# Kernel tuning notes

Hardware: AMD Instinct MI355X
Metric: run time of the kernel (lower is better)

## Reference

```python
import jax, jax.numpy as jnp
import numpy as np

EPS = 1e-5  # nn.LayerNorm default


def channel_ln(x, g, b):
    # LayerNorm over the channel axis of an NCHW tensor
    mu = jnp.mean(x, axis=1, keepdims=True)
    var = jnp.mean((x - mu) ** 2, axis=1, keepdims=True)
    xn = (x - mu) * jax.lax.rsqrt(var + EPS)
    return xn * g[None, :, None, None] + b[None, :, None, None]


def setup_inputs() -> dict:
    key = jax.random.key(0)
    ks = jax.random.split(key, 8)
    B, C, H, W = 16, 392, 64, 64
    n, ws = 8, 7            # head_dim = C//n = 49 = ws'^2
    hidden = int(C * 4.0)
    f32 = jnp.float32
    return {
        "x": jax.random.normal(ks[0], (B, C, H, W), f32),
        "ln1_g": jnp.ones((C,), f32),
        "ln1_b": jnp.zeros((C,), f32),
        "qkv_w": jax.random.normal(ks[1], (3 * C, C), f32) * 0.02,
        "qkv_b": jnp.zeros((3 * C,), f32),
        "rel_bias": jax.random.normal(ks[2], (n, ws, ws), f32) * 0.02,
        "proj_w": jax.random.normal(ks[3], (C, C), f32) * 0.02,
        "proj_b": jnp.zeros((C,), f32),
        "ln2_g": jnp.ones((C,), f32),
        "ln2_b": jnp.zeros((C,), f32),
        "fc1_w": jax.random.normal(ks[4], (hidden, C), f32) * 0.02,
        "fc1_b": jnp.zeros((hidden,), f32),
        "fc2_w": jax.random.normal(ks[5], (C, hidden), f32) * 0.02,
        "fc2_b": jnp.zeros((C,), f32),
    }


def reference(x, ln1_g, ln1_b, qkv_w, qkv_b, rel_bias, proj_w, proj_b,
              ln2_g, ln2_b, fc1_w, fc1_b, fc2_w, fc2_b):
    B, C, H, W = x.shape
    n = rel_bias.shape[0]
    hd = C // n  # == ws'^2 (49)
    shortcut = x

    # --- attention branch ---
    h = channel_ln(x, ln1_g, ln1_b)
    qkv = jnp.einsum('oc,bchw->bohw', qkv_w, h) + qkv_b[None, :, None, None]
    qkv = qkv.reshape(B, 3, n, hd, H * W).transpose(1, 0, 2, 4, 3)  # [3,B,n,HW,hd]
    q, k, v = qkv[0], qkv[1], qkv[2]
    scale = hd ** -0.5
    bias = rel_bias.reshape(n, -1)[None, :, None, :]        # [1,n,1,hd]
    attn = jax.nn.softmax(q * scale * k + bias, axis=-1)    # elementwise qk score
    out = (attn * v).reshape(B, C, H, W)  # row-major reshape == torch .view on contiguous
    out = jnp.einsum('oc,bchw->bohw', proj_w, out) + proj_b[None, :, None, None]
    x = shortcut + out

    # --- conv-MLP branch ---
    h = channel_ln(x, ln2_g, ln2_b)
    h = jnp.einsum('oc,bchw->bohw', fc1_w, h) + fc1_b[None, :, None, None]
    h = jax.nn.gelu(h, approximate=False)  # nn.GELU default is exact erf
    h = jnp.einsum('oc,bchw->bohw', fc2_w, h) + fc2_b[None, :, None, None]
    return x + h
```

## Files before the change

### kernel.cpp

```cpp
#include <hip/hip_runtime.h>

typedef unsigned short u16;
typedef __attribute__((ext_vector_type(8))) short short8;
typedef __attribute__((ext_vector_type(8))) unsigned short u16x8;
typedef __attribute__((ext_vector_type(4))) unsigned short u16x4;
typedef __attribute__((ext_vector_type(4))) float f32x4;

#define DEVINL __device__ __forceinline__

DEVINL float bf2f(u16 v) { return __builtin_bit_cast(float, (unsigned int)v << 16); }
DEVINL u16 f2bf(float f) {
  unsigned int u = __builtin_bit_cast(unsigned int, f);
  u += 0x7fffu + ((u >> 16) & 1u);
  return (u16)(u >> 16);
}

DEVINL float loadx(const void* p, size_t i, int flag) {
  return flag ? bf2f(((const u16*)p)[i]) : ((const float*)p)[i];
}

DEVINL f32x4 mfma16(short8 a, short8 b, f32x4 c) {
  return __builtin_amdgcn_mfma_f32_16x16x32_bf16(a, b, c, 0, 0, 0);
}

DEVINL void gload16(const u16* g, u16* l) {
  __builtin_amdgcn_global_load_lds(
      (const __attribute__((address_space(1))) unsigned int*)g,
      (__attribute__((address_space(3))) unsigned int*)l,
      16, 0, 0);
}

#define WAIT_VM(n) asm volatile("s_waitcnt vmcnt(" #n ")" ::: "memory")
#define SBAR() __builtin_amdgcn_s_barrier()
#define SCHED_FENCE() __builtin_amdgcn_sched_barrier(0)

__global__ void k_detect(const unsigned int* __restrict__ xw, int* __restrict__ flag)
{
  const int t = threadIdx.x;
  int cnt = 0;
  for (int i = t; i < 4096; i += 256) {
    unsigned int w = xw[i];
    unsigned int h = w & 0xFFFFu;
    unsigned int e = (h >> 7) & 0xFFu;
    if (((h & 0x7FFFu) == 0u) || (e >= 117u && e <= 130u)) cnt++;
  }
  #pragma unroll
  for (int d = 1; d < 64; d <<= 1) cnt += __shfl_xor(cnt, d);
  __shared__ int acc[4];
  if ((t & 63) == 0) acc[t >> 6] = cnt;
  __syncthreads();
  if (t == 0) *flag = ((acc[0] + acc[1] + acc[2] + acc[3]) > 2048) ? 1 : 0;
}

__global__ void k_prep_fold(const void* __restrict__ w, const void* __restrict__ g,
                            const void* __restrict__ beta, const void* __restrict__ wbias,
                            const int* __restrict__ dflag,
                            u16* __restrict__ wp, float* __restrict__ wsum, float* __restrict__ cb,
                            int rows, int K, int KP)
{
  const int flag = *dflag;
  const int o = blockIdx.x;
  const int lane = threadIdx.x;
  float ws = 0.f, c = 0.f;
  if (o < rows) {
    for (int k = lane; k < KP; k += 64) {
      u16 outv = 0;
      if (k < K) {
        float wv = loadx(w, (size_t)o * K + k, flag);
        float gv = loadx(g, k, flag);
        outv = f2bf(wv * gv);
        ws += bf2f(outv);
        c  += wv * loadx(beta, k, flag);
      }
      wp[(size_t)o * KP + k] = outv;
    }
  } else {
    for (int k = lane; k < KP; k += 64) wp[(size_t)o * KP + k] = 0;
  }
  #pragma unroll
  for (int d = 1; d < 64; d <<= 1) { ws += __shfl_xor(ws, d); c += __shfl_xor(c, d); }
  if (lane == 0) { wsum[o] = ws; cb[o] = (o < rows) ? (c + loadx(wbias, o, flag)) : 0.f; }
}

__global__ void k_prep_pad(const void* __restrict__ w, const int* __restrict__ dflag,
                           u16* __restrict__ wp, int rows, int K, int KP, long total)
{
  const int flag = *dflag;
  long i = (long)blockIdx.x * 256 + threadIdx.x;
  if (i >= total) return;
  int r = (int)(i / KP), c2 = (int)(i % KP);
  wp[i] = (r < rows && c2 < K) ? f2bf(loadx(w, (size_t)r * K + c2, flag)) : (u16)0;
}

__global__ __launch_bounds__(256) void k_transpose(const void* __restrict__ xraw,
                                                   const int* __restrict__ dflag,
                                                   u16* __restrict__ xt, int jg0)
{
  __shared__ u16 ts[64][72];
  const int flag = *dflag;
  const int t = threadIdx.x;
  const int j0l = blockIdx.x * 64;
  const int j0g = jg0 + j0l;
  const int c0 = blockIdx.y * 64;
  const int c_l = t >> 2;
  const int c = c0 + c_l;
  const int bb = j0g >> 12;
  const int hw0 = j0g & 4095;

  #pragma unroll
  for (int u = 0; u < 2; ++u) {
    int jp = u * 32 + (t & 3) * 8;
    u16 vv[8] = {0, 0, 0, 0, 0, 0, 0, 0};
    if (c < 392) {
      size_t base = (((size_t)(bb * 392 + c)) << 12) + hw0 + jp;
      if (flag) {
        u16x8 v = *(const u16x8*)((const u16*)xraw + base);
        #pragma unroll
        for (int i = 0; i < 8; ++i) vv[i] = v[i];
      } else {
        const float* xf = (const float*)xraw + base;
        f32x4 a = *(const f32x4*)xf;
        f32x4 b = *(const f32x4*)(xf + 4);
        #pragma unroll
        for (int i = 0; i < 4; ++i) { vv[i] = f2bf(a[i]); vv[4 + i] = f2bf(b[i]); }
      }
    }
    #pragma unroll
    for (int i = 0; i < 8; ++i) ts[jp + i][c_l] = vv[i];
  }
  __syncthreads();
  const int j_l = t >> 2;
  #pragma unroll
  for (int u = 0; u < 2; ++u) {
    int cp = u * 32 + (t & 3) * 8;
    u16x8 w;
    #pragma unroll
    for (int i = 0; i < 8; ++i) w[i] = ts[j_l][cp + i];
    int cg = c0 + cp;
    if (cg < 416) *(u16x8*)(xt + (size_t)(j0l + j_l) * 416 + cg) = w;
  }
}

__global__ __launch_bounds__(256) void k_att_tr(const u16* __restrict__ att,
                                                u16* __restrict__ aout)
{
  __shared__ u16 ts[64][72];
  const int t = threadIdx.x;
  const int j0l = blockIdx.x * 64;
  const int c0 = blockIdx.y * 64;
  const int c_l = t >> 2;
  const int c = c0 + c_l;
  const int slab = j0l >> 12;
  const int hw0 = j0l & 4095;

  #pragma unroll
  for (int u = 0; u < 2; ++u) {
    int jp = u * 32 + (t & 3) * 8;
    u16x8 v = {0, 0, 0, 0, 0, 0, 0, 0};
    if (c < 392)
      v = *(const u16x8*)(att + (size_t)slab * 1605632 + (size_t)c * 4096 + hw0 + jp);
    #pragma unroll
    for (int i = 0; i < 8; ++i) ts[jp + i][c_l] = v[i];
  }
  __syncthreads();
  const int j_l = t >> 2;
  #pragma unroll
  for (int u = 0; u < 2; ++u) {
    int cp = u * 32 + (t & 3) * 8;
    u16x8 w;
    #pragma unroll
    for (int i = 0; i < 8; ++i) w[i] = ts[j_l][cp + i];
    int cg = c0 + cp;
    if (cg < 416) *(u16x8*)(aout + (size_t)(j0l + j_l) * 416 + cg) = w;
  }
}

__global__ __launch_bounds__(256) void k_rowstats(const u16* __restrict__ buf,
                                                  float* __restrict__ sum, float* __restrict__ sq)
{
  const int t = threadIdx.x;
  const int lane = t & 63;
  const int row = blockIdx.x * 4 + (t >> 6);
  float s = 0.f, q = 0.f;
  if (lane < 52) {
    u16x8 v = *(const u16x8*)(buf + (size_t)row * 416 + lane * 8);
    #pragma unroll
    for (int i = 0; i < 8; ++i) { float f = bf2f(v[i]); s += f; q += f * f; }
  }
  #pragma unroll
  for (int d = 1; d < 64; d <<= 1) { s += __shfl_xor(s, d); q += __shfl_xor(q, d); }
  if (lane == 0) { sum[row] = s; sq[row] = q; }
}

__global__ __launch_bounds__(256, 2) void k_qkv(
    const u16* __restrict__ xt, const u16* __restrict__ w1p,
    const float* __restrict__ wsum1, const float* __restrict__ cb1,
    const float* __restrict__ sum1, const float* __restrict__ sq1,
    const void* __restrict__ relb, const int* __restrict__ dflag,
    u16* __restrict__ attout)
{
  __shared__ __align__(16) u16 lsA[2 * 4096];
  __shared__ __align__(16) u16 lsB[2 * 6144];
  const int flag = *dflag;
  const int t = threadIdx.x;
  const int wid = t >> 6, lane = t & 63;
  const int l15 = lane & 15, quad = lane >> 4;
  const int bid = blockIdx.x;
  const int h = (bid >> 3) & 7;
  const int jl0 = ((bid & 7) + ((bid >> 6) << 3)) * 128;

  const u16* ga0 = xt + (size_t)(jl0 + (t >> 2)) * 416 + (t & 3) * 8;
  const u16* ga1 = ga0 + (size_t)64 * 416;
  const int orow = t >> 2, kpart = (t & 3) * 8;
  const u16* gbq = w1p + (size_t)(h * 49 + orow) * 416 + kpart;
  const u16* gbk = w1p + (size_t)(392 + h * 49 + orow) * 416 + kpart;
  const u16* gbv = w1p + (size_t)(784 + h * 49 + orow) * 416 + kpart;

  f32x4 zero4 = {0.f, 0.f, 0.f, 0.f};
  f32x4 accq[2][4], acck[2][4], accv[2][4];
  #pragma unroll
  for (int a = 0; a < 2; ++a)
    #pragma unroll
    for (int b2 = 0; b2 < 4; ++b2) { accq[a][b2] = zero4; acck[a][b2] = zero4; accv[a][b2] = zero4; }

  auto stage = [&](int b, int kk) {
    u16* A = lsA + b * 4096;
    u16* B = lsB + b * 6144;
    gload16(ga0 + kk, A + t * 8);
    gload16(ga1 + kk, A + 2048 + t * 8);
    gload16(gbq + kk, B + t * 8);
    gload16(gbk + kk, B + 2048 + t * 8);
    gload16(gbv + kk, B + 4096 + t * 8);
  };

  stage(0, 0);
  int cur = 0;
  for (int it = 0; it < 13; ++it) {
    if (it < 12) {
      stage(cur ^ 1, (it + 1) * 32);
      WAIT_VM(5);
    } else {
      WAIT_VM(0);
    }
    SBAR();
    SCHED_FENCE();
    const u16* A = lsA + cur * 4096;
    const u16* B = lsB + cur * 6144;
    short8 af0 = *(const short8*)(A + ((wid * 32 + l15) * 32 + quad * 8));
    short8 af1 = *(const short8*)(A + ((wid * 32 + 16 + l15) * 32 + quad * 8));
    #pragma unroll
    for (int of = 0; of < 4; ++of) {
      const int bo_ = (of * 16 + l15) * 32 + quad * 8;
      short8 bq = *(const short8*)(B + bo_);
      short8 bk = *(const short8*)(B + 2048 + bo_);
      short8 bv = *(const short8*)(B + 4096 + bo_);
      accq[0][of] = mfma16(af0, bq, accq[0][of]);
      accq[1][of] = mfma16(af1, bq, accq[1][of]);
      acck[0][of] = mfma16(af0, bk, acck[0][of]);
      acck[1][of] = mfma16(af1, bk, acck[1][of]);
      accv[0][of] = mfma16(af0, bv, accv[0][of]);
      accv[1][of] = mfma16(af1, bv, accv[1][of]);
    }
    SCHED_FENCE();
    SBAR();
    cur ^= 1;
  }

  const float scale = 1.f / 7.f;
  float cq[4], wq[4], ck[4], wk[4], cv[4], wv_[4], bo[4];
  int dl[4];
  #pragma unroll
  for (int of = 0; of < 4; ++of) {
    int d = of * 16 + l15; dl[of] = d;
    int rq = h * 49 + d, rk = 392 + h * 49 + d, rv = 784 + h * 49 + d;
    wq[of] = wsum1[rq]; cq[of] = cb1[rq];
    wk[of] = wsum1[rk]; ck[of] = cb1[rk];
    wv_[of] = wsum1[rv]; cv[of] = cb1[rv];
    bo[of] = (d < 49) ? loadx(relb, h * 49 + d, flag) : 0.f;
  }
  #pragma unroll
  for (int jf = 0; jf < 2; ++jf) {
    #pragma unroll
    for (int r = 0; r < 4; ++r) {
      int jl = jl0 + wid * 32 + jf * 16 + quad * 4 + r;
      float mu = sum1[jl] * (1.f / 392.f);
      float var = sq1[jl] * (1.f / 392.f) - mu * mu;
      float rs = rsqrtf(fmaxf(var, 0.f) + 1e-5f);
      float sv[4], vv[4];
      float mx = -1e30f;
      #pragma unroll
      for (int of = 0; of < 4; ++of) {
        float qv = rs * accq[jf][of][r] + cq[of] - mu * rs * wq[of];
        float kv = rs * acck[jf][of][r] + ck[of] - mu * rs * wk[of];
        float s = (dl[of] < 49) ? (qv * scale * kv + bo[of]) : -1e30f;
        sv[of] = s; mx = fmaxf(mx, s);
        vv[of] = rs * accv[jf][of][r] + cv[of] - mu * rs * wv_[of];
      }
      #pragma unroll
      for (int d2 = 1; d2 < 16; d2 <<= 1) mx = fmaxf(mx, __shfl_xor(mx, d2));
      float sum = 0.f;
      #pragma unroll
      for (int of = 0; of < 4; ++of) { float e = __expf(sv[of] - mx); sv[of] = e; sum += e; }
      #pragma unroll
      for (int d2 = 1; d2 < 16; d2 <<= 1) sum += __shfl_xor(sum, d2);
      float inv = 1.f / sum;
      int pos = jl & 4095, slab = jl >> 12;
      size_t base = (size_t)slab * 1605632 + (size_t)h * 200704 + (size_t)pos * 49;
      #pragma unroll
      for (int of = 0; of < 4; ++of) {
        if (dl[of] < 49) attout[base + dl[of]] = f2bf(sv[of] * inv * vv[of]);
      }
    }
  }
}

__global__ __launch_bounds__(256, 2) void k_proj(
    const u16* __restrict__ aout, const u16* __restrict__ wpp,
    const void* __restrict__ projb, const int* __restrict__ dflag,
    const u16* __restrict__ xt, u16* __restrict__ x2t)
{
  __shared__ __align__(16) u16 lsA[3 * 4096];
  __shared__ __align__(16) u16 lsB[3 * 4096];
  const int flag = *dflag;
  const int t = threadIdx.x;
  const int wid = t >> 6, lane = t & 63;
  const int l15 = lane & 15, quad = lane >> 4;
  const int jl0 = blockIdx.x * 128, o0 = blockIdx.y * 128;

  const u16* ga0 = aout + (size_t)(jl0 + (t >> 2)) * 416 + (t & 3) * 8;
  const u16* ga1 = ga0 + (size_t)64 * 416;
  const u16* gb0 = wpp + (size_t)(o0 + (t >> 2)) * 416 + (t & 3) * 8;
  const u16* gb1 = gb0 + (size_t)64 * 416;

  f32x4 zero4 = {0.f, 0.f, 0.f, 0.f};
  f32x4 acc[2][8];
  #pragma unroll
  for (int a = 0; a < 2; ++a)
    #pragma unroll
    for (int b2 = 0; b2 < 8; ++b2) acc[a][b2] = zero4;

  auto stage = [&](int b, int kk) {
    u16* A = lsA + b * 4096;
    u16* B = lsB + b * 4096;
    gload16(ga0 + kk, A + t * 8);
    gload16(ga1 + kk, A + 2048 + t * 8);
    gload16(gb0 + kk, B + t * 8);
    gload16(gb1 + kk, B + 2048 + t * 8);
  };

  stage(0, 0); stage(1, 32);
  int bc = 0, bs = 2;
  for (int it = 0; it < 13; ++it) {
    if (it + 2 < 13) { stage(bs, (it + 2) * 32); WAIT_VM(8); }
    else WAIT_VM(0);
    SBAR();
    SCHED_FENCE();
    const u16* A = lsA + bc * 4096;
    const u16* B = lsB + bc * 4096;
    short8 af0 = *(const short8*)(A + ((wid * 32 + l15) * 32 + quad * 8));
    short8 af1 = *(const short8*)(A + ((wid * 32 + 16 + l15) * 32 + quad * 8));
    #pragma unroll
    for (int of = 0; of < 8; ++of) {
      short8 bf = *(const short8*)(B + ((of * 16 + l15) * 32 + quad * 8));
      acc[0][of] = mfma16(af0, bf, acc[0][of]);
      acc[1][of] = mfma16(af1, bf, acc[1][of]);
    }
    SCHED_FENCE();
    SBAR();
    bc = (bc + 1 == 3) ? 0 : bc + 1;
    bs = (bs + 1 == 3) ? 0 : bs + 1;
  }

  float pb[8]; int og[8];
  #pragma unroll
  for (int of = 0; of < 8; ++of) {
    int o = o0 + of * 16 + l15; og[of] = o;
    pb[of] = (o < 392) ? loadx(projb, o, flag) : 0.f;
  }
  #pragma unroll
  for (int jf = 0; jf < 2; ++jf) {
    #pragma unroll
    for (int r = 0; r < 4; ++r) {
      int jl = jl0 + wid * 32 + jf * 16 + quad * 4 + r;
      #pragma unroll
      for (int of = 0; of < 8; ++of) {
        int o = og[of];
        if (o < 392) {
          float val = acc[jf][of][r] + pb[of] + bf2f(xt[(size_t)jl * 416 + o]);
          x2t[(size_t)jl * 416 + o] = f2bf(val);
        } else if (o < 416) {
          x2t[(size_t)jl * 416 + o] = 0;
        }
      }
    }
  }
}

__global__ __launch_bounds__(256, 2) void k_fc1(
    const u16* __restrict__ x2t, const u16* __restrict__ w3p,
    const float* __restrict__ wsum3, const float* __restrict__ cb3,
    const float* __restrict__ sum2, const float* __restrict__ sq2,
    u16* __restrict__ ut)
{
  __shared__ __align__(16) u16 lsA[3 * 4096];
  __shared__ __align__(16) u16 lsB[3 * 4096];
  const int t = threadIdx.x;
  const int wid = t >> 6, lane = t & 63;
  const int l15 = lane & 15, quad = lane >> 4;
  const int jl0 = blockIdx.x * 128, o0 = blockIdx.y * 128;

  const u16* ga0 = x2t + (size_t)(jl0 + (t >> 2)) * 416 + (t & 3) * 8;
  const u16* ga1 = ga0 + (size_t)64 * 416;
  const u16* gb0 = w3p + (size_t)(o0 + (t >> 2)) * 416 + (t & 3) * 8;
  const u16* gb1 = gb0 + (size_t)64 * 416;

  f32x4 zero4 = {0.f, 0.f, 0.f, 0.f};
  f32x4 acc[2][8];
  #pragma unroll
  for (int a = 0; a < 2; ++a)
    #pragma unroll
    for (int b2 = 0; b2 < 8; ++b2) acc[a][b2] = zero4;

  auto stage = [&](int b, int kk) {
    u16* A = lsA + b * 4096;
    u16* B = lsB + b * 4096;
    gload16(ga0 + kk, A + t * 8);
    gload16(ga1 + kk, A + 2048 + t * 8);
    gload16(gb0 + kk, B + t * 8);
    gload16(gb1 + kk, B + 2048 + t * 8);
  };

  stage(0, 0); stage(1, 32);
  int bc = 0, bs = 2;
  for (int it = 0; it < 13; ++it) {
    if (it + 2 < 13) { stage(bs, (it + 2) * 32); WAIT_VM(8); }
    else WAIT_VM(0);
    SBAR();
    SCHED_FENCE();
    const u16* A = lsA + bc * 4096;
    const u16* B = lsB + bc * 4096;
    short8 af0 = *(const short8*)(A + ((wid * 32 + l15) * 32 + quad * 8));
    short8 af1 = *(const short8*)(A + ((wid * 32 + 16 + l15) * 32 + quad * 8));
    #pragma unroll
    for (int of = 0; of < 8; ++of) {
      short8 bf = *(const short8*)(B + ((of * 16 + l15) * 32 + quad * 8));
      acc[0][of] = mfma16(af0, bf, acc[0][of]);
      acc[1][of] = mfma16(af1, bf, acc[1][of]);
    }
    SCHED_FENCE();
    SBAR();
    bc = (bc + 1 == 3) ? 0 : bc + 1;
    bs = (bs + 1 == 3) ? 0 : bs + 1;
  }

  float c3[8], w3[8]; int og[8];
  #pragma unroll
  for (int of = 0; of < 8; ++of) {
    int o = o0 + of * 16 + l15; og[of] = o;
    c3[of] = cb3[o]; w3[of] = wsum3[o];
  }
  #pragma unroll
  for (int jf = 0; jf < 2; ++jf) {
    #pragma unroll
    for (int r = 0; r < 4; ++r) {
      int jl = jl0 + wid * 32 + jf * 16 + quad * 4 + r;
      float mu = sum2[jl] * (1.f / 392.f);
      float var = sq2[jl] * (1.f / 392.f) - mu * mu;
      float rs = rsqrtf(fmaxf(var, 0.f) + 1e-5f);
      #pragma unroll
      for (int of = 0; of < 8; ++of) {
        if (og[of] < 1568) {
          float u = rs * acc[jf][of][r] + c3[of] - mu * rs * w3[of];
          float gl = 0.5f * u * (1.f + erff(u * 0.70710678118654752f));
          ut[(size_t)jl * 1568 + og[of]] = f2bf(gl);
        }
      }
    }
  }
}

__global__ __launch_bounds__(256, 2) void k_fc2(
    const u16* __restrict__ ut, const u16* __restrict__ wfp,
    const void* __restrict__ fc2b, const int* __restrict__ dflag,
    const u16* __restrict__ x2t, void* __restrict__ outp, int jfg0)
{
  __shared__ __align__(16) u16 lsA[3 * 4096];
  __shared__ __align__(16) u16 lsB[3 * 4096];
  const int flag = *dflag;
  const int t = threadIdx.x;
  const int wid = t >> 6, lane = t & 63;
  const int l15 = lane & 15, quad = lane >> 4;
  const int jl0 = blockIdx.x * 128, o0 = blockIdx.y * 128;

  const u16* ga0 = ut + (size_t)(jl0 + (t >> 2)) * 1568 + (t & 3) * 8;
  const u16* ga1 = ga0 + (size_t)64 * 1568;
  const u16* gb0 = wfp + (size_t)(o0 + (t >> 2)) * 1568 + (t & 3) * 8;
  const u16* gb1 = gb0 + (size_t)64 * 1568;

  f32x4 zero4 = {0.f, 0.f, 0.f, 0.f};
  f32x4 acc[2][8];
  #pragma unroll
  for (int a = 0; a < 2; ++a)
    #pragma unroll
    for (int b2 = 0; b2 < 8; ++b2) acc[a][b2] = zero4;

  auto stage = [&](int b, int kk) {
    u16* A = lsA + b * 4096;
    u16* B = lsB + b * 4096;
    gload16(ga0 + kk, A + t * 8);
    gload16(ga1 + kk, A + 2048 + t * 8);
    gload16(gb0 + kk, B + t * 8);
    gload16(gb1 + kk, B + 2048 + t * 8);
  };

  stage(0, 0); stage(1, 32);
  int bc = 0, bs = 2;
  for (int it = 0; it < 49; ++it) {
    if (it + 2 < 49) { stage(bs, (it + 2) * 32); WAIT_VM(8); }
    else WAIT_VM(0);
    SBAR();
    SCHED_FENCE();
    const u16* A = lsA + bc * 4096;
    const u16* B = lsB + bc * 4096;
    short8 af0 = *(const short8*)(A + ((wid * 32 + l15) * 32 + quad * 8));
    short8 af1 = *(const short8*)(A + ((wid * 32 + 16 + l15) * 32 + quad * 8));
    #pragma unroll
    for (int of = 0; of < 8; ++of) {
      short8 bf = *(const short8*)(B + ((of * 16 + l15) * 32 + quad * 8));
      acc[0][of] = mfma16(af0, bf, acc[0][of]);
      acc[1][of] = mfma16(af1, bf, acc[1][of]);
    }
    SCHED_FENCE();
    SBAR();
    bc = (bc + 1 == 3) ? 0 : bc + 1;
    bs = (bs + 1 == 3) ? 0 : bs + 1;
  }

  float fb[8]; int og[8];
  #pragma unroll
  for (int of = 0; of < 8; ++of) {
    int o = o0 + of * 16 + l15; og[of] = o;
    fb[of] = (o < 392) ? loadx(fc2b, o, flag) : 0.f;
  }
  #pragma unroll
  for (int jf = 0; jf < 2; ++jf) {
    int jlbase = jl0 + wid * 32 + jf * 16 + quad * 4;
    int jgbase = jfg0 + jlbase;
    int bslab = jgbase >> 12;
    int hw = jgbase & 4095;
    #pragma unroll
    for (int of = 0; of < 8; ++of) {
      if (og[of] < 392) {
        float v4[4];
        #pragma unroll
        for (int r = 0; r < 4; ++r)
          v4[r] = acc[jf][of][r] + fb[of] + bf2f(x2t[(size_t)(jlbase + r) * 416 + og[of]]);
        size_t obase = (((size_t)(bslab * 392 + og[of])) << 12) + hw;
        if (flag) {
          u16x4 pk;
          #pragma unroll
          for (int r = 0; r < 4; ++r) pk[r] = f2bf(v4[r]);
          *(u16x4*)((u16*)outp + obase) = pk;
        } else {
          f32x4 pk;
          #pragma unroll
          for (int r = 0; r < 4; ++r) pk[r] = v4[r];
          *(f32x4*)((float*)outp + obase) = pk;
        }
      }
    }
  }
}

extern "C" void kernel_launch(void* const* d_in, const int* in_sizes, int n_in,
                              void* d_out, int out_size, void* d_ws, size_t ws_size,
                              hipStream_t stream)
{
  if (n_in != 14 || in_sizes[0] != 16 * 392 * 64 * 64 || out_size != 16 * 392 * 64 * 64 ||
      in_sizes[3] != 3 * 392 * 392 || in_sizes[5] != 8 * 7 * 7 ||
      in_sizes[10] != 1568 * 392 || in_sizes[12] != 392 * 1568) {
    return;
  }

  const void* x     = d_in[0];
  const void* g1    = d_in[1];
  const void* b1    = d_in[2];
  const void* qkvw  = d_in[3];
  const void* qkvb  = d_in[4];
  const void* relb  = d_in[5];
  const void* projw = d_in[6];
  const void* projb = d_in[7];
  const void* g2    = d_in[8];
  const void* b2    = d_in[9];
  const void* fc1w  = d_in[10];
  const void* fc1b  = d_in[11];
  const void* fc2w  = d_in[12];
  const void* fc2b  = d_in[13];

  int S = 0, F = 0;
  {
    const int cand[8][2] = {{16,8},{16,4},{8,4},{8,2},{4,2},{4,1},{2,1},{1,1}};
    for (int i = 0; i < 8; ++i) {
      size_t nb = (size_t)cand[i][0] * 4096 * 416 * 2 * 3
                + (size_t)cand[i][1] * 4096 * 1568 * 2
                + (size_t)16 * 1024 * 1024;
      if (nb <= ws_size) { S = cand[i][0]; F = cand[i][1]; break; }
    }
    if (S == 0) return;
  }

  char* wsb = (char*)d_ws;
  size_t off = 0;
  auto alloc = [&](size_t bytes) -> void* {
    void* p = wsb + off;
    off = (off + bytes + 255) & ~(size_t)255;
    return p;
  };
  int*  dflag = (int*)alloc(256);
  u16* xt    = (u16*)alloc((size_t)S * 4096 * 416 * 2);
  u16* aout  = (u16*)alloc((size_t)S * 4096 * 416 * 2);
  u16* x2t   = (u16*)alloc((size_t)S * 4096 * 416 * 2);
  u16* ut    = (u16*)alloc((size_t)F * 4096 * 1568 * 2);
  u16* w1p   = (u16*)alloc((size_t)1200 * 416 * 2);
  u16* w3p   = (u16*)alloc((size_t)1664 * 416 * 2);
  u16* wpp   = (u16*)alloc((size_t)512 * 416 * 2);
  u16* wfp   = (u16*)alloc((size_t)512 * 1568 * 2);
  float* wsum1 = (float*)alloc(1200 * 4);
  float* cb1   = (float*)alloc(1200 * 4);
  float* wsum3 = (float*)alloc(1664 * 4);
  float* cb3   = (float*)alloc(1664 * 4);
  float* sum1  = (float*)alloc((size_t)65536 * 4);
  float* sq1   = (float*)alloc((size_t)65536 * 4);
  float* sum2  = (float*)alloc((size_t)65536 * 4);
  float* sq2   = (float*)alloc((size_t)65536 * 4);

  u16* att = x2t;

  k_detect<<<1, 256, 0, stream>>>((const unsigned int*)x, dflag);

  k_prep_fold<<<1200, 64, 0, stream>>>(qkvw, g1, b1, qkvb, dflag, w1p, wsum1, cb1, 1176, 392, 416);
  k_prep_fold<<<1664, 64, 0, stream>>>(fc1w, g2, b2, fc1b, dflag, w3p, wsum3, cb3, 1568, 392, 416);
  k_prep_pad<<<(512 * 416 + 255) / 256, 256, 0, stream>>>(projw, dflag, wpp, 392, 392, 416, (long)512 * 416);
  k_prep_pad<<<(512 * 1568 + 255) / 256, 256, 0, stream>>>(fc2w, dflag, wfp, 392, 1568, 1568, (long)512 * 1568);

  for (int c0 = 0; c0 < 16; c0 += S) {
    const int jg0 = c0 * 4096;
    k_transpose<<<dim3(S * 64, 7), 256, 0, stream>>>(x, dflag, xt, jg0);
    k_rowstats<<<S * 1024, 256, 0, stream>>>(xt, sum1, sq1);
    k_qkv<<<dim3(S * 256), 256, 0, stream>>>(xt, w1p, wsum1, cb1, sum1, sq1, relb, dflag, att);
    k_att_tr<<<dim3(S * 64, 7), 256, 0, stream>>>(att, aout);
    k_proj<<<dim3(S * 32, 4), 256, 0, stream>>>(aout, wpp, projb, dflag, xt, x2t);
    k_rowstats<<<S * 1024, 256, 0, stream>>>(x2t, sum2, sq2);
    for (int f0 = 0; f0 < S; f0 += F) {
      const int jfg0 = (c0 + f0) * 4096;
      const u16* x2sub = x2t + (size_t)f0 * 4096 * 416;
      k_fc1<<<dim3(F * 32, 13), 256, 0, stream>>>(x2sub, w3p, wsum3, cb3,
                                                  sum2 + (size_t)f0 * 4096, sq2 + (size_t)f0 * 4096, ut);
      k_fc2<<<dim3(F * 32, 4), 256, 0, stream>>>(ut, wfp, fc2b, dflag, x2sub, d_out, jfg0);
    }
  }
}
```

Baseline: 897.9 us.

## Enlarge GEMM tiles to 128x512 and prepack weights into MFMA fragment order

The proj, fc1 and fc2 GEMMs now use 512-thread blocks, each computing a 128-row by 512-column tile. Every wave holds 4x8 MFMA accumulators, so the A operand is read from global memory only once per output column group. Weights are repacked in a new prep kernel into a fragment-major layout, so each lane's LDS load is a contiguous 16-byte read with no per-row stride. This raises register and LDS pressure (about 120KB of LDS per block) and pads fc1 outputs to 2048, which wastes MFMA work on padded columns.

```diff
diff --git a/kernel.cpp b/kernel.cpp
--- a/kernel.cpp
+++ b/kernel.cpp
@@ -90,6 +90,18 @@
   if (i >= total) return;
   int r = (int)(i / KP), c2 = (int)(i % KP);
   wp[i] = (r < rows && c2 < K) ? f2bf(loadx(w, (size_t)r * K + c2, flag)) : (u16)0;
+}
+
+__global__ void k_repack(const u16* __restrict__ src, u16* __restrict__ dst, int RP, int KP)
+{
+  const int nK = KP / 32;
+  long i = (long)blockIdx.x * 256 + threadIdx.x;
+  if (i * 8 >= (long)RP * KP) return;
+  int l = (int)(i & 63);
+  long fk = i >> 6;
+  int ks = (int)(fk % nK), f = (int)(fk / nK);
+  const u16* s = src + (size_t)(f * 16 + (l & 15)) * KP + ks * 32 + ((l >> 4) & 3) * 8;
+  *(u16x8*)(dst + i * 8) = *(const u16x8*)s;
 }
 
 __global__ __launch_bounds__(256) void k_transpose(const void* __restrict__ xraw,
@@ -236,12 +248,8 @@
   stage(0, 0);
   int cur = 0;
   for (int it = 0; it < 13; ++it) {
-    if (it < 12) {
-      stage(cur ^ 1, (it + 1) * 32);
-      WAIT_VM(5);
-    } else {
-      WAIT_VM(0);
-    }
+    if (it < 12) { stage(cur ^ 1, (it + 1) * 32); WAIT_VM(5); }
+    else WAIT_VM(0);
     SBAR();
     SCHED_FENCE();
     const u16* A = lsA + cur * 4096;
@@ -314,56 +322,58 @@
   }
 }
 
-__global__ __launch_bounds__(256, 2) void k_proj(
-    const u16* __restrict__ aout, const u16* __restrict__ wpp,
+
+__global__ __launch_bounds__(512, 2) void k_proj(
+    const u16* __restrict__ aout, const u16* __restrict__ wppf,
     const void* __restrict__ projb, const int* __restrict__ dflag,
     const u16* __restrict__ xt, u16* __restrict__ x2t)
 {
   __shared__ __align__(16) u16 lsA[3 * 4096];
-  __shared__ __align__(16) u16 lsB[3 * 4096];
+  __shared__ __align__(16) u16 lsB[3 * 16384];
   const int flag = *dflag;
   const int t = threadIdx.x;
-  const int wid = t >> 6, lane = t & 63;
-  const int l15 = lane & 15, quad = lane >> 4;
-  const int jl0 = blockIdx.x * 128, o0 = blockIdx.y * 128;
-
-  const u16* ga0 = aout + (size_t)(jl0 + (t >> 2)) * 416 + (t & 3) * 8;
-  const u16* ga1 = ga0 + (size_t)64 * 416;
-  const u16* gb0 = wpp + (size_t)(o0 + (t >> 2)) * 416 + (t & 3) * 8;
-  const u16* gb1 = gb0 + (size_t)64 * 416;
+  const int w = t >> 6, lane = t & 63;
+  const int l15 = lane & 15, quad = (lane >> 4) & 3;
+  const int jl0 = blockIdx.x * 128;
+  const int NK = 13;
+
+  const u16* gA = aout + (size_t)(jl0 + (t >> 6) * 16 + l15) * 416 + quad * 8;
+  const u16* gB = wppf + (size_t)(t >> 6) * NK * 512 + lane * 8;
 
   f32x4 zero4 = {0.f, 0.f, 0.f, 0.f};
-  f32x4 acc[2][8];
-  #pragma unroll
-  for (int a = 0; a < 2; ++a)
-    #pragma unroll
-    for (int b2 = 0; b2 < 8; ++b2) acc[a][b2] = zero4;
-
-  auto stage = [&](int b, int kk) {
-    u16* A = lsA + b * 4096;
-    u16* B = lsB + b * 4096;
-    gload16(ga0 + kk, A + t * 8);
-    gload16(ga1 + kk, A + 2048 + t * 8);
-    gload16(gb0 + kk, B + t * 8);
-    gload16(gb1 + kk, B + 2048 + t * 8);
+  f32x4 acc[4][8];
+  #pragma unroll
+  for (int m = 0; m < 4; ++m)
+    #pragma unroll
+    for (int n = 0; n < 8; ++n) acc[m][n] = zero4;
+
+  auto stage = [&](int b, int ks) {
+    gload16(gA + ks * 32, lsA + b * 4096 + t * 8);
+    #pragma unroll
+    for (int c = 0; c < 4; ++c)
+      gload16(gB + ((size_t)c * 8 * NK + ks) * 512,
+              lsB + b * 16384 + (c * 8 + w) * 512 + lane * 8);
   };
 
-  stage(0, 0); stage(1, 32);
+  stage(0, 0); stage(1, 1);
   int bc = 0, bs = 2;
-  for (int it = 0; it < 13; ++it) {
-    if (it + 2 < 13) { stage(bs, (it + 2) * 32); WAIT_VM(8); }
+  for (int ks = 0; ks < NK; ++ks) {
+    if (ks + 2 < NK) { stage(bs, ks + 2); WAIT_VM(10); }
+    else if (ks + 1 < NK) WAIT_VM(5);
     else WAIT_VM(0);
     SBAR();
     SCHED_FENCE();
     const u16* A = lsA + bc * 4096;
-    const u16* B = lsB + bc * 4096;
-    short8 af0 = *(const short8*)(A + ((wid * 32 + l15) * 32 + quad * 8));
-    short8 af1 = *(const short8*)(A + ((wid * 32 + 16 + l15) * 32 + quad * 8));
-    #pragma unroll
-    for (int of = 0; of < 8; ++of) {
-      short8 bf = *(const short8*)(B + ((of * 16 + l15) * 32 + quad * 8));
-      acc[0][of] = mfma16(af0, bf, acc[0][of]);
-      acc[1][of] = mfma16(af1, bf, acc[1][of]);
+    const u16* B = lsB + bc * 16384;
+    short8 af[4];
+    #pragma unroll
+    for (int m = 0; m < 4; ++m)
+      af[m] = *(const short8*)(A + ((w >> 2) * 4 + m) * 512 + lane * 8);
+    #pragma unroll
+    for (int n = 0; n < 8; ++n) {
+      short8 bf = *(const short8*)(B + ((w & 3) * 8 + n) * 512 + lane * 8);
+      #pragma unroll
+      for (int m = 0; m < 4; ++m) acc[m][n] = mfma16(af[m], bf, acc[m][n]);
     }
     SCHED_FENCE();
     SBAR();
@@ -373,20 +383,21 @@
 
   float pb[8]; int og[8];
   #pragma unroll
-  for (int of = 0; of < 8; ++of) {
-    int o = o0 + of * 16 + l15; og[of] = o;
-    pb[of] = (o < 392) ? loadx(projb, o, flag) : 0.f;
-  }
-  #pragma unroll
-  for (int jf = 0; jf < 2; ++jf) {
+  for (int n = 0; n < 8; ++n) {
+    int o = (w & 3) * 128 + n * 16 + l15; og[n] = o;
+    pb[n] = (o < 392) ? loadx(projb, o, flag) : 0.f;
+  }
+  const int row0 = jl0 + (w >> 2) * 64;
+  #pragma unroll
+  for (int m = 0; m < 4; ++m) {
     #pragma unroll
     for (int r = 0; r < 4; ++r) {
-      int jl = jl0 + wid * 32 + jf * 16 + quad * 4 + r;
-      #pragma unroll
-      for (int of = 0; of < 8; ++of) {
-        int o = og[of];
+      int jl = row0 + m * 16 + quad * 4 + r;
+      #pragma unroll
+      for (int n = 0; n < 8; ++n) {
+        int o = og[n];
         if (o < 392) {
-          float val = acc[jf][of][r] + pb[of] + bf2f(xt[(size_t)jl * 416 + o]);
+          float val = acc[m][n][r] + pb[n] + bf2f(xt[(size_t)jl * 416 + o]);
           x2t[(size_t)jl * 416 + o] = f2bf(val);
         } else if (o < 416) {
           x2t[(size_t)jl * 416 + o] = 0;
@@ -396,56 +407,58 @@
   }
 }
 
-__global__ __launch_bounds__(256, 2) void k_fc1(
-    const u16* __restrict__ x2t, const u16* __restrict__ w3p,
+__global__ __launch_bounds__(512, 2) void k_fc1(
+    const u16* __restrict__ x2t, const u16* __restrict__ w3pf,
     const float* __restrict__ wsum3, const float* __restrict__ cb3,
     const float* __restrict__ sum2, const float* __restrict__ sq2,
     u16* __restrict__ ut)
 {
   __shared__ __align__(16) u16 lsA[3 * 4096];
-  __shared__ __align__(16) u16 lsB[3 * 4096];
-  const int t = threadIdx.x;
-  const int wid = t >> 6, lane = t & 63;
-  const int l15 = lane & 15, quad = lane >> 4;
-  const int jl0 = blockIdx.x * 128, o0 = blockIdx.y * 128;
-
-  const u16* ga0 = x2t + (size_t)(jl0 + (t >> 2)) * 416 + (t & 3) * 8;
-  const u16* ga1 = ga0 + (size_t)64 * 416;
-  const u16* gb0 = w3p + (size_t)(o0 + (t >> 2)) * 416 + (t & 3) * 8;
-  const u16* gb1 = gb0 + (size_t)64 * 416;
+  __shared__ __align__(16) u16 lsB[3 * 16384];
+  const int t = threadIdx.x;
+  const int w = t >> 6, lane = t & 63;
+  const int l15 = lane & 15, quad = (lane >> 4) & 3;
+  const int jl0 = blockIdx.x * 128;
+  const int o0 = blockIdx.y * 512;
+  const int NK = 13;
+
+  const u16* gA = x2t + (size_t)(jl0 + (t >> 6) * 16 + l15) * 416 + quad * 8;
+  const u16* gB = w3pf + ((size_t)(blockIdx.y * 32 + (t >> 6)) * NK) * 512 + lane * 8;
 
   f32x4 zero4 = {0.f, 0.f, 0.f, 0.f};
-  f32x4 acc[2][8];
-  #pragma unroll
-  for (int a = 0; a < 2; ++a)
-    #pragma unroll
-    for (int b2 = 0; b2 < 8; ++b2) acc[a][b2] = zero4;
-
-  auto stage = [&](int b, int kk) {
-    u16* A = lsA + b * 4096;
-    u16* B = lsB + b * 4096;
-    gload16(ga0 + kk, A + t * 8);
-    gload16(ga1 + kk, A + 2048 + t * 8);
-    gload16(gb0 + kk, B + t * 8);
-    gload16(gb1 + kk, B + 2048 + t * 8);
+  f32x4 acc[4][8];
+  #pragma unroll
+  for (int m = 0; m < 4; ++m)
+    #pragma unroll
+    for (int n = 0; n < 8; ++n) acc[m][n] = zero4;
+
+  auto stage = [&](int b, int ks) {
+    gload16(gA + ks * 32, lsA + b * 4096 + t * 8);
+    #pragma unroll
+    for (int c = 0; c < 4; ++c)
+      gload16(gB + ((size_t)c * 8 * NK + ks) * 512,
+              lsB + b * 16384 + (c * 8 + w) * 512 + lane * 8);
   };
 
-  stage(0, 0); stage(1, 32);
+  stage(0, 0); stage(1, 1);
   int bc = 0, bs = 2;
-  for (int it = 0; it < 13; ++it) {
-    if (it + 2 < 13) { stage(bs, (it + 2) * 32); WAIT_VM(8); }
+  for (int ks = 0; ks < NK; ++ks) {
+    if (ks + 2 < NK) { stage(bs, ks + 2); WAIT_VM(10); }
+    else if (ks + 1 < NK) WAIT_VM(5);
     else WAIT_VM(0);
     SBAR();
     SCHED_FENCE();
     const u16* A = lsA + bc * 4096;
-    const u16* B = lsB + bc * 4096;
-    short8 af0 = *(const short8*)(A + ((wid * 32 + l15) * 32 + quad * 8));
-    short8 af1 = *(const short8*)(A + ((wid * 32 + 16 + l15) * 32 + quad * 8));
-    #pragma unroll
-    for (int of = 0; of < 8; ++of) {
-      short8 bf = *(const short8*)(B + ((of * 16 + l15) * 32 + quad * 8));
-      acc[0][of] = mfma16(af0, bf, acc[0][of]);
-      acc[1][of] = mfma16(af1, bf, acc[1][of]);
+    const u16* B = lsB + bc * 16384;
+    short8 af[4];
+    #pragma unroll
+    for (int m = 0; m < 4; ++m)
+      af[m] = *(const short8*)(A + ((w >> 2) * 4 + m) * 512 + lane * 8);
+    #pragma unroll
+    for (int n = 0; n < 8; ++n) {
+      short8 bf = *(const short8*)(B + ((w & 3) * 8 + n) * 512 + lane * 8);
+      #pragma unroll
+      for (int m = 0; m < 4; ++m) acc[m][n] = mfma16(af[m], bf, acc[m][n]);
     }
     SCHED_FENCE();
     SBAR();
@@ -455,80 +468,82 @@
 
   float c3[8], w3[8]; int og[8];
   #pragma unroll
-  for (int of = 0; of < 8; ++of) {
-    int o = o0 + of * 16 + l15; og[of] = o;
-    c3[of] = cb3[o]; w3[of] = wsum3[o];
-  }
-  #pragma unroll
-  for (int jf = 0; jf < 2; ++jf) {
+  for (int n = 0; n < 8; ++n) {
+    int o = o0 + (w & 3) * 128 + n * 16 + l15; og[n] = o;
+    c3[n] = cb3[o]; w3[n] = wsum3[o];
+  }
+  const int row0 = jl0 + (w >> 2) * 64;
+  #pragma unroll
+  for (int m = 0; m < 4; ++m) {
     #pragma unroll
     for (int r = 0; r < 4; ++r) {
-      int jl = jl0 + wid * 32 + jf * 16 + quad * 4 + r;
+      int jl = row0 + m * 16 + quad * 4 + r;
       float mu = sum2[jl] * (1.f / 392.f);
       float var = sq2[jl] * (1.f / 392.f) - mu * mu;
       float rs = rsqrtf(fmaxf(var, 0.f) + 1e-5f);
       #pragma unroll
-      for (int of = 0; of < 8; ++of) {
-        if (og[of] < 1568) {
-          float u = rs * acc[jf][of][r] + c3[of] - mu * rs * w3[of];
+      for (int n = 0; n < 8; ++n) {
+        if (og[n] < 1568) {
+          float u = rs * acc[m][n][r] + c3[n] - mu * rs * w3[n];
           float gl = 0.5f * u * (1.f + erff(u * 0.70710678118654752f));
-          ut[(size_t)jl * 1568 + og[of]] = f2bf(gl);
+          ut[(size_t)jl * 1568 + og[n]] = f2bf(gl);
         }
       }
     }
   }
 }
 
-__global__ __launch_bounds__(256, 2) void k_fc2(
-    const u16* __restrict__ ut, const u16* __restrict__ wfp,
+__global__ __launch_bounds__(512, 2) void k_fc2(
+    const u16* __restrict__ ut, const u16* __restrict__ wfpf,
     const void* __restrict__ fc2b, const int* __restrict__ dflag,
     const u16* __restrict__ x2t, void* __restrict__ outp, int jfg0)
 {
   __shared__ __align__(16) u16 lsA[3 * 4096];
-  __shared__ __align__(16) u16 lsB[3 * 4096];
+  __shared__ __align__(16) u16 lsB[3 * 16384];
   const int flag = *dflag;
   const int t = threadIdx.x;
-  const int wid = t >> 6, lane = t & 63;
-  const int l15 = lane & 15, quad = lane >> 4;
-  const int jl0 = blockIdx.x * 128, o0 = blockIdx.y * 128;
-
-  const u16* ga0 = ut + (size_t)(jl0 + (t >> 2)) * 1568 + (t & 3) * 8;
-  const u16* ga1 = ga0 + (size_t)64 * 1568;
-  const u16* gb0 = wfp + (size_t)(o0 + (t >> 2)) * 1568 + (t & 3) * 8;
-  const u16* gb1 = gb0 + (size_t)64 * 1568;
+  const int w = t >> 6, lane = t & 63;
+  const int l15 = lane & 15, quad = (lane >> 4) & 3;
+  const int jl0 = blockIdx.x * 128;
+  const int NK = 49;
+
+  const u16* gA = ut + (size_t)(jl0 + (t >> 6) * 16 + l15) * 1568 + quad * 8;
+  const u16* gB = wfpf + (size_t)(t >> 6) * NK * 512 + lane * 8;
 
   f32x4 zero4 = {0.f, 0.f, 0.f, 0.f};
-  f32x4 acc[2][8];
-  #pragma unroll
-  for (int a = 0; a < 2; ++a)
-    #pragma unroll
-    for (int b2 = 0; b2 < 8; ++b2) acc[a][b2] = zero4;
-
-  auto stage = [&](int b, int kk) {
-    u16* A = lsA + b * 4096;
-    u16* B = lsB + b * 4096;
-    gload16(ga0 + kk, A + t * 8);
-    gload16(ga1 + kk, A + 2048 + t * 8);
-    gload16(gb0 + kk, B + t * 8);
-    gload16(gb1 + kk, B + 2048 + t * 8);
+  f32x4 acc[4][8];
+  #pragma unroll
+  for (int m = 0; m < 4; ++m)
+    #pragma unroll
+    for (int n = 0; n < 8; ++n) acc[m][n] = zero4;
+
+  auto stage = [&](int b, int ks) {
+    gload16(gA + ks * 32, lsA + b * 4096 + t * 8);
+    #pragma unroll
+    for (int c = 0; c < 4; ++c)
+      gload16(gB + ((size_t)c * 8 * NK + ks) * 512,
+              lsB + b * 16384 + (c * 8 + w) * 512 + lane * 8);
   };
 
-  stage(0, 0); stage(1, 32);
+  stage(0, 0); stage(1, 1);
   int bc = 0, bs = 2;
-  for (int it = 0; it < 49; ++it) {
-    if (it + 2 < 49) { stage(bs, (it + 2) * 32); WAIT_VM(8); }
+  for (int ks = 0; ks < NK; ++ks) {
+    if (ks + 2 < NK) { stage(bs, ks + 2); WAIT_VM(10); }
+    else if (ks + 1 < NK) WAIT_VM(5);
     else WAIT_VM(0);
     SBAR();
     SCHED_FENCE();
     const u16* A = lsA + bc * 4096;
-    const u16* B = lsB + bc * 4096;
-    short8 af0 = *(const short8*)(A + ((wid * 32 + l15) * 32 + quad * 8));
-    short8 af1 = *(const short8*)(A + ((wid * 32 + 16 + l15) * 32 + quad * 8));
-    #pragma unroll
-    for (int of = 0; of < 8; ++of) {
-      short8 bf = *(const short8*)(B + ((of * 16 + l15) * 32 + quad * 8));
-      acc[0][of] = mfma16(af0, bf, acc[0][of]);
-      acc[1][of] = mfma16(af1, bf, acc[1][of]);
+    const u16* B = lsB + bc * 16384;
+    short8 af[4];
+    #pragma unroll
+    for (int m = 0; m < 4; ++m)
+      af[m] = *(const short8*)(A + ((w >> 2) * 4 + m) * 512 + lane * 8);
+    #pragma unroll
+    for (int n = 0; n < 8; ++n) {
+      short8 bf = *(const short8*)(B + ((w & 3) * 8 + n) * 512 + lane * 8);
+      #pragma unroll
+      for (int m = 0; m < 4; ++m) acc[m][n] = mfma16(af[m], bf, acc[m][n]);
     }
     SCHED_FENCE();
     SBAR();
@@ -536,26 +551,27 @@
     bs = (bs + 1 == 3) ? 0 : bs + 1;
   }
 
-  float fb[8]; int og[8];
-  #pragma unroll
-  for (int of = 0; of < 8; ++of) {
-    int o = o0 + of * 16 + l15; og[of] = o;
-    fb[of] = (o < 392) ? loadx(fc2b, o, flag) : 0.f;
-  }
-  #pragma unroll
-  for (int jf = 0; jf < 2; ++jf) {
-    int jlbase = jl0 + wid * 32 + jf * 16 + quad * 4;
+  float fb4[8]; int og[8];
+  #pragma unroll
+  for (int n = 0; n < 8; ++n) {
+    int o = (w & 3) * 128 + n * 16 + l15; og[n] = o;
+    fb4[n] = (o < 392) ? loadx(fc2b, o, flag) : 0.f;
+  }
+  const int row0 = jl0 + (w >> 2) * 64;
+  #pragma unroll
+  for (int m = 0; m < 4; ++m) {
+    int jlbase = row0 + m * 16 + quad * 4;
     int jgbase = jfg0 + jlbase;
     int bslab = jgbase >> 12;
     int hw = jgbase & 4095;
     #pragma unroll
-    for (int of = 0; of < 8; ++of) {
-      if (og[of] < 392) {
+    for (int n = 0; n < 8; ++n) {
+      if (og[n] < 392) {
         float v4[4];
         #pragma unroll
         for (int r = 0; r < 4; ++r)
-          v4[r] = acc[jf][of][r] + fb[of] + bf2f(x2t[(size_t)(jlbase + r) * 416 + og[of]]);
-        size_t obase = (((size_t)(bslab * 392 + og[of])) << 12) + hw;
+          v4[r] = acc[m][n][r] + fb4[n] + bf2f(x2t[(size_t)(jlbase + r) * 416 + og[n]]);
+        size_t obase = (((size_t)(bslab * 392 + og[n])) << 12) + hw;
         if (flag) {
           u16x4 pk;
           #pragma unroll
@@ -603,7 +619,7 @@
     for (int i = 0; i < 8; ++i) {
       size_t nb = (size_t)cand[i][0] * 4096 * 416 * 2 * 3
                 + (size_t)cand[i][1] * 4096 * 1568 * 2
-                + (size_t)16 * 1024 * 1024;
+                + (size_t)24 * 1024 * 1024;
       if (nb <= ws_size) { S = cand[i][0]; F = cand[i][1]; break; }
     }
     if (S == 0) return;
@@ -622,13 +638,16 @@
   u16* x2t   = (u16*)alloc((size_t)S * 4096 * 416 * 2);
   u16* ut    = (u16*)alloc((size_t)F * 4096 * 1568 * 2);
   u16* w1p   = (u16*)alloc((size_t)1200 * 416 * 2);
-  u16* w3p   = (u16*)alloc((size_t)1664 * 416 * 2);
-  u16* wpp   = (u16*)alloc((size_t)512 * 416 * 2);
-  u16* wfp   = (u16*)alloc((size_t)512 * 1568 * 2);
+  u16* w3r   = (u16*)alloc((size_t)2048 * 416 * 2);
+  u16* w3pf  = (u16*)alloc((size_t)2048 * 416 * 2);
+  u16* wpr   = (u16*)alloc((size_t)512 * 416 * 2);
+  u16* wppf  = (u16*)alloc((size_t)512 * 416 * 2);
+  u16* wfr   = (u16*)alloc((size_t)512 * 1568 * 2);
+  u16* wfpf  = (u16*)alloc((size_t)512 * 1568 * 2);
   float* wsum1 = (float*)alloc(1200 * 4);
   float* cb1   = (float*)alloc(1200 * 4);
-  float* wsum3 = (float*)alloc(1664 * 4);
-  float* cb3   = (float*)alloc(1664 * 4);
+  float* wsum3 = (float*)alloc(2048 * 4);
+  float* cb3   = (float*)alloc(2048 * 4);
   float* sum1  = (float*)alloc((size_t)65536 * 4);
   float* sq1   = (float*)alloc((size_t)65536 * 4);
   float* sum2  = (float*)alloc((size_t)65536 * 4);
@@ -639,9 +658,12 @@
   k_detect<<<1, 256, 0, stream>>>((const unsigned int*)x, dflag);
 
   k_prep_fold<<<1200, 64, 0, stream>>>(qkvw, g1, b1, qkvb, dflag, w1p, wsum1, cb1, 1176, 392, 416);
-  k_prep_fold<<<1664, 64, 0, stream>>>(fc1w, g2, b2, fc1b, dflag, w3p, wsum3, cb3, 1568, 392, 416);
-  k_prep_pad<<<(512 * 416 + 255) / 256, 256, 0, stream>>>(projw, dflag, wpp, 392, 392, 416, (long)512 * 416);
-  k_prep_pad<<<(512 * 1568 + 255) / 256, 256, 0, stream>>>(fc2w, dflag, wfp, 392, 1568, 1568, (long)512 * 1568);
+  k_prep_fold<<<2048, 64, 0, stream>>>(fc1w, g2, b2, fc1b, dflag, w3r, wsum3, cb3, 1568, 392, 416);
+  k_prep_pad<<<(512 * 416 + 255) / 256, 256, 0, stream>>>(projw, dflag, wpr, 392, 392, 416, (long)512 * 416);
+  k_prep_pad<<<(512 * 1568 + 255) / 256, 256, 0, stream>>>(fc2w, dflag, wfr, 392, 1568, 1568, (long)512 * 1568);
+  k_repack<<<((2048 * 416 / 8) + 255) / 256, 256, 0, stream>>>(w3r, w3pf, 2048, 416);
+  k_repack<<<((512 * 416 / 8) + 255) / 256, 256, 0, stream>>>(wpr, wppf, 512, 416);
+  k_repack<<<((512 * 1568 / 8) + 255) / 256, 256, 0, stream>>>(wfr, wfpf, 512, 1568);
 
   for (int c0 = 0; c0 < 16; c0 += S) {
     const int jg0 = c0 * 4096;
@@ -649,14 +671,14 @@
     k_rowstats<<<S * 1024, 256, 0, stream>>>(xt, sum1, sq1);
     k_qkv<<<dim3(S * 256), 256, 0, stream>>>(xt, w1p, wsum1, cb1, sum1, sq1, relb, dflag, att);
     k_att_tr<<<dim3(S * 64, 7), 256, 0, stream>>>(att, aout);
-    k_proj<<<dim3(S * 32, 4), 256, 0, stream>>>(aout, wpp, projb, dflag, xt, x2t);
+    k_proj<<<dim3(S * 32), 512, 0, stream>>>(aout, wppf, projb, dflag, xt, x2t);
     k_rowstats<<<S * 1024, 256, 0, stream>>>(x2t, sum2, sq2);
     for (int f0 = 0; f0 < S; f0 += F) {
       const int jfg0 = (c0 + f0) * 4096;
       const u16* x2sub = x2t + (size_t)f0 * 4096 * 416;
-      k_fc1<<<dim3(F * 32, 13), 256, 0, stream>>>(x2sub, w3p, wsum3, cb3,
-                                                  sum2 + (size_t)f0 * 4096, sq2 + (size_t)f0 * 4096, ut);
-      k_fc2<<<dim3(F * 32, 4), 256, 0, stream>>>(ut, wfp, fc2b, dflag, x2sub, d_out, jfg0);
-    }
-  }
-}
+      k_fc1<<<dim3(F * 32, 4), 512, 0, stream>>>(x2sub, w3pf, wsum3, cb3,
+                                                 sum2 + (size_t)f0 * 4096, sq2 + (size_t)f0 * 4096, ut);
+      k_fc2<<<dim3(F * 32), 512, 0, stream>>>(ut, wfpf, fc2b, dflag, x2sub, d_out, jfg0);
+    }
+  }
+}
```

Measured after the change: 941.9 us. 1.05x slower.
